# Kernel optimization log

Measured on AMD Instinct MI355X. Metric: run time of the kernel, lower is better.

## Reference

```python
import jax, jax.numpy as jnp
import numpy as np

EPS = 1e-12
NEG_SLOPE = 0.2

def _normalize(x):
    # F.normalize(x, p=2, dim=1)
    n = jnp.sqrt(jnp.sum(x * x, axis=-1, keepdims=True))
    return x / jnp.maximum(n, EPS)

def setup_inputs() -> dict:
    key = jax.random.key(0)
    ks = jax.random.split(key, 10)
    n_users, n_items, n_entities = 100000, 50000, 200000
    n_rel, n_edges, n_inter, n_hops, d = 32, 2000000, 1000000, 2, 64
    return {
        "user_emb": jax.random.normal(ks[0], (n_users, d), jnp.float32) * 0.1,
        "entity_emb": jax.random.normal(ks[1], (n_entities, d), jnp.float32) * 0.1,
        "rel_weight": jax.random.normal(ks[2], (n_rel, d), jnp.float32) * 0.1,
        "gate1_w": jax.random.normal(ks[3], (n_hops, d, d), jnp.float32) * 0.1,
        "gate2_w": jax.random.normal(ks[4], (n_hops, d, d), jnp.float32) * 0.1,
        "head": jax.random.randint(ks[5], (n_edges,), 0, n_entities, jnp.int32),
        "tail": jax.random.randint(ks[6], (n_edges,), 0, n_entities, jnp.int32),
        "edge_type": jax.random.randint(ks[7], (n_edges,), 0, n_rel, jnp.int32),
        "mat_row": jax.random.randint(ks[8], (n_inter,), 0, n_users, jnp.int32),
        "mat_col": jax.random.randint(ks[9], (n_inter,), 0, n_items, jnp.int32),
    }

def reference(user_emb, entity_emb, rel_weight, gate1_w, gate2_w,
              head, tail, edge_type, mat_row, mat_col):
    n_users = user_emb.shape[0]
    n_entities = entity_emb.shape[0]
    n_items = 50000
    n_hops = gate1_w.shape[0]

    entity_res = entity_emb
    user_res = user_emb
    for i in range(n_hops):
        # KG aggregate: gather-scale-scatter over KG triples
        msg = entity_emb[tail] * rel_weight[edge_type]          # [E, d]
        entity_agg = jax.ops.segment_sum(msg, head, num_segments=n_entities)
        # CF aggregate: user -> item
        item_neigh = user_emb[mat_row] * rel_weight[0]          # [I, d]
        i_u_agg = jax.ops.segment_sum(item_neigh, mat_col, num_segments=n_items)
        # gated fusion of KG-side and CF-side item embeddings
        ea_items = entity_agg[:n_items]
        gi = jax.nn.leaky_relu(ea_items @ gate1_w[i].T + i_u_agg @ gate2_w[i].T,
                               negative_slope=NEG_SLOPE)
        item_fusion = gi * ea_items + (1.0 - gi) * i_u_agg
        # sparse mm with binary user-item matrix == segment_sum over rows
        user_agg = jax.ops.segment_sum(item_fusion[mat_col], mat_row,
                                       num_segments=n_users)
        entity_emb = jnp.concatenate([item_fusion, entity_agg[n_items:]], axis=0)
        entity_emb = _normalize(entity_emb)
        user_emb = _normalize(user_agg)
        entity_res = entity_res + entity_emb
        user_res = user_res + user_emb
    # concatenate outputs: [n_entities + n_users, d]
    return jnp.concatenate([entity_res, user_res], axis=0)
```

## Files before the change

kernel.cpp:

```cpp
#include <hip/hip_runtime.h>
#include <hip/hip_bf16.h>

#define D 64
#define N_USERS 100000
#define N_ITEMS 50000
#define N_ENT   200000
#define EPS 1e-12f
#define CHUNK 4096
#define NBINP 512
#define CAP   8192

typedef unsigned short u16;

template<int MODE> struct Cfg;
template<> struct Cfg<0> { static constexpr int SHIFT = 9; static constexpr int NSEG = N_ENT;   };
template<> struct Cfg<1> { static constexpr int SHIFT = 7; static constexpr int NSEG = N_ITEMS; };
template<> struct Cfg<2> { static constexpr int SHIFT = 8; static constexpr int NSEG = N_USERS; };
template<int MODE> constexpr int nbin_of() {
  return (Cfg<MODE>::NSEG + (1 << Cfg<MODE>::SHIFT) - 1) >> Cfg<MODE>::SHIFT;
}

__device__ __forceinline__ float bf2f(u16 u) {
  return __uint_as_float(((unsigned)u) << 16);
}
__device__ __forceinline__ u16 f2bf(float f) {
  unsigned u = __float_as_uint(f);
  unsigned r = (u + 0x7FFFu + ((u >> 16) & 1u)) >> 16;
  return (u16)r;
}
__device__ __forceinline__ float wave_rsqnorm(float v) {
  float ss = v * v;
#pragma unroll
  for (int m = 1; m < 64; m <<= 1) ss += __shfl_xor(ss, m);
  return 1.f / fmaxf(sqrtf(ss), EPS);
}
__device__ __forceinline__ float bcast(float v, int k) {
  return __uint_as_float(__builtin_amdgcn_readlane(__float_as_uint(v), k));
}

__global__ __launch_bounds__(256) void init_embed(
    const float* __restrict__ ent, const float* __restrict__ usr,
    float* __restrict__ out_ent, float* __restrict__ out_usr,
    u16* __restrict__ ent_bf, u16* __restrict__ usr_bf) {
  int i = blockIdx.x * 256 + threadIdx.x;
  if (i < N_ENT * D) {
    float v = ent[i];
    out_ent[i] = v;
    ent_bf[i] = f2bf(v);
  }
  if (i < N_USERS * D) {
    float v = usr[i];
    out_usr[i] = v;
    usr_bf[i] = f2bf(v);
  }
}

__global__ __launch_bounds__(256) void scan_block(
    const int* __restrict__ in, int* __restrict__ out,
    int* __restrict__ bsum, int n) {
  __shared__ int sm[256];
  int tid = threadIdx.x;
  int i = blockIdx.x * 256 + tid;
  int v = (i < n) ? in[i] : 0;
  sm[tid] = v;
  __syncthreads();
  for (int ofs = 1; ofs < 256; ofs <<= 1) {
    int t = (tid >= ofs) ? sm[tid - ofs] : 0;
    __syncthreads();
    sm[tid] += t;
    __syncthreads();
  }
  if (i < n) out[i] = sm[tid] - v;
  if (tid == 255) bsum[blockIdx.x] = sm[255];
}

__global__ __launch_bounds__(1024) void scan_top(int* __restrict__ bsum, int nb) {
  __shared__ int sm[1024];
  int tid = threadIdx.x;
  int v = (tid < nb) ? bsum[tid] : 0;
  sm[tid] = v;
  __syncthreads();
  for (int ofs = 1; ofs < 1024; ofs <<= 1) {
    int t = (tid >= ofs) ? sm[tid - ofs] : 0;
    __syncthreads();
    sm[tid] += t;
    __syncthreads();
  }
  if (tid < nb) bsum[tid] = sm[tid] - v;
}

__global__ __launch_bounds__(256) void scan_addv(
    int* __restrict__ out, const int* __restrict__ bsum, int n) {
  int i = blockIdx.x * 256 + threadIdx.x;
  if (i < n) out[i] += bsum[blockIdx.x];
}

template<int MODE>
__global__ __launch_bounds__(256) void p1_hist(
    const int* __restrict__ keys, int n, int* __restrict__ bc, int nblk) {
  constexpr int SHIFT = Cfg<MODE>::SHIFT;
  constexpr int NBIN = nbin_of<MODE>();
  __shared__ int h[NBINP];
  int tid = threadIdx.x;
  h[tid] = 0; h[tid + 256] = 0;
  __syncthreads();
  int base = blockIdx.x * CHUNK;
  int end = min(base + CHUNK, n);
  for (int i = base + tid; i < end; i += 256)
    atomicAdd(&h[keys[i] >> SHIFT], 1);
  __syncthreads();
  for (int b = tid; b < NBIN; b += 256)
    bc[b * nblk + blockIdx.x] = h[b];
}

template<int MODE>
__global__ __launch_bounds__(256) void p1_scatter(
    const int* __restrict__ keys, const int* __restrict__ pa,
    const int* __restrict__ pb, int n, const int* __restrict__ sbc, int nblk,
    int2* __restrict__ out) {
  constexpr int SHIFT = Cfg<MODE>::SHIFT;
  constexpr int NBIN = nbin_of<MODE>();
  __shared__ int h[NBINP];
  __shared__ int cur[NBINP];
  __shared__ int bb[NBINP];
  __shared__ int2 staged[CHUNK];
  __shared__ int dstA[CHUNK];
  int tid = threadIdx.x;
  h[tid] = 0; h[tid + 256] = 0;
  __syncthreads();
  int base = blockIdx.x * CHUNK;
  int end = min(base + CHUNK, n);
  for (int i = base + tid; i < end; i += 256)
    atomicAdd(&h[keys[i] >> SHIFT], 1);
  __syncthreads();
  int o0 = h[tid], o1 = h[tid + 256];
  for (int ofs = 1; ofs < NBINP; ofs <<= 1) {
    int v0 = (tid >= ofs) ? h[tid - ofs] : 0;
    int v1 = (tid + 256 >= ofs) ? h[tid + 256 - ofs] : 0;
    __syncthreads();
    h[tid] += v0; h[tid + 256] += v1;
    __syncthreads();
  }
  int e0 = h[tid] - o0, e1 = h[tid + 256] - o1;
  cur[tid] = e0; cur[tid + 256] = e1;
  if (tid < NBIN)        bb[tid] = sbc[tid * nblk + blockIdx.x] - e0;
  if (tid + 256 < NBIN)  bb[tid + 256] = sbc[(tid + 256) * nblk + blockIdx.x] - e1;
  __syncthreads();
  for (int i = base + tid; i < end; i += 256) {
    int k = keys[i];
    int bin = k >> SHIFT;
    int payload;
    if constexpr (MODE == 0) payload = pa[i] | (pb[i] << 24);
    else                     payload = pa[i];
    int lp = atomicAdd(&cur[bin], 1);
    staged[lp] = make_int2(k, payload);
    dstA[lp] = bb[bin] + lp;
  }
  __syncthreads();
  int cnt = end - base;
  for (int t = tid; t < cnt; t += 256) out[dstA[t]] = staged[t];
}

template<int MODE>
__global__ __launch_bounds__(256) void p2_sort(
    const int2* __restrict__ binned, const int* __restrict__ sbc, int nblk,
    int n, int* __restrict__ vals, int* __restrict__ off) {
  constexpr int SHIFT = Cfg<MODE>::SHIFT;
  constexpr int NSEG = Cfg<MODE>::NSEG;
  constexpr int SEGBIN = 1 << SHIFT;
  constexpr int NBIN = nbin_of<MODE>();
  __shared__ int h[NBINP];
  __shared__ int cur[NBINP];
  __shared__ int staged[CAP];
  int tid = threadIdx.x;
  int b = blockIdx.x;
  int start = sbc[b * nblk];
  int endp = (b == NBIN - 1) ? n : sbc[(b + 1) * nblk];
  int cnt = endp - start;
  h[tid] = 0; h[tid + 256] = 0;
  __syncthreads();
  int segbase = b << SHIFT;
  for (int t = tid; t < cnt; t += 256)
    atomicAdd(&h[binned[start + t].x - segbase], 1);
  __syncthreads();
  int o0 = h[tid], o1 = h[tid + 256];
  for (int ofs = 1; ofs < NBINP; ofs <<= 1) {
    int v0 = (tid >= ofs) ? h[tid - ofs] : 0;
    int v1 = (tid + 256 >= ofs) ? h[tid + 256 - ofs] : 0;
    __syncthreads();
    h[tid] += v0; h[tid + 256] += v1;
    __syncthreads();
  }
  int e0 = h[tid] - o0, e1 = h[tid + 256] - o1;
  if (tid < SEGBIN && segbase + tid < NSEG) off[segbase + tid] = start + e0;
  if (tid + 256 < SEGBIN && segbase + tid + 256 < NSEG)
    off[segbase + tid + 256] = start + e1;
  if (b == NBIN - 1 && tid == 0) off[NSEG] = n;
  cur[tid] = e0; cur[tid + 256] = e1;
  __syncthreads();
  if (cnt <= CAP) {
    for (int t = tid; t < cnt; t += 256) {
      int2 e = binned[start + t];
      int lp = atomicAdd(&cur[e.x - segbase], 1);
      staged[lp] = e.y;
    }
    __syncthreads();
    for (int t = tid; t < cnt; t += 256) vals[start + t] = staged[t];
  } else {
    for (int t = tid; t < cnt; t += 256) {
      int2 e = binned[start + t];
      int lp = atomicAdd(&cur[e.x - segbase], 1);
      vals[start + lp] = e.y;
    }
  }
}

__global__ __launch_bounds__(256) void kg_gather(
    const u16* __restrict__ ent, const float* __restrict__ relw,
    const int* __restrict__ off, const int* __restrict__ pk,
    float* __restrict__ ea_items, u16* __restrict__ ent_next,
    float* __restrict__ res) {
  int h = blockIdx.x * 4 + (threadIdx.x >> 6);
  if (h >= N_ENT) return;
  int lane = threadIdx.x & 63;
  int b = off[h], e = off[h + 1];
  float acc = 0.f;
  for (int j0 = b; j0 < e; j0 += 64) {
    int cnt = min(64, e - j0);
    int p = (j0 + lane < e) ? pk[j0 + lane] : 0;
    int jj = 0;
    for (; jj + 8 <= cnt; jj += 8) {
      u16 uv[8];
      float rw[8];
#pragma unroll
      for (int k = 0; k < 8; ++k) {
        int q = __shfl(p, jj + k);
        uv[k] = ent[(q & 0xFFFFFF) * D + lane];
        rw[k] = relw[(((unsigned)q) >> 24) * D + lane];
      }
#pragma unroll
      for (int k = 0; k < 8; ++k) acc += bf2f(uv[k]) * rw[k];
    }
    for (; jj < cnt; ++jj) {
      int q = __shfl(p, jj);
      acc += bf2f(ent[(q & 0xFFFFFF) * D + lane]) *
             relw[(((unsigned)q) >> 24) * D + lane];
    }
  }
  int o = h * D + lane;
  if (h < N_ITEMS) {
    ea_items[o] = acc;
  } else {
    float nv = acc * wave_rsqnorm(acc);
    ent_next[o] = f2bf(nv);
    res[o] += nv;
  }
}

__device__ __forceinline__ float segsum_idx_bf(
    const int* __restrict__ il, int b, int e, int lane,
    const u16* __restrict__ tab) {
  float acc = 0.f;
  for (int j0 = b; j0 < e; j0 += 64) {
    int cnt = min(64, e - j0);
    int p = (j0 + lane < e) ? il[j0 + lane] : 0;
    int jj = 0;
    for (; jj + 8 <= cnt; jj += 8) {
      u16 uv[8];
#pragma unroll
      for (int k = 0; k < 8; ++k) {
        int q = __shfl(p, jj + k);
        uv[k] = tab[q * D + lane];
      }
#pragma unroll
      for (int k = 0; k < 8; ++k) acc += bf2f(uv[k]);
    }
    for (; jj < cnt; ++jj) acc += bf2f(tab[__shfl(p, jj) * D + lane]);
  }
  return acc;
}

__global__ __launch_bounds__(256) void inter_gather(
    const u16* __restrict__ usr_bf, const float* __restrict__ relw,
    const int* __restrict__ off, const int* __restrict__ vr,
    float* __restrict__ iu) {
  int c = blockIdx.x * 4 + (threadIdx.x >> 6);
  if (c >= N_ITEMS) return;
  int lane = threadIdx.x & 63;
  int b = off[c], e = off[c + 1];
  float acc = segsum_idx_bf(vr, b, e, lane, usr_bf);
  iu[c * D + lane] = acc * relw[lane];
}

__global__ __launch_bounds__(256) void fuse_items(
    const float* __restrict__ ea_items, const float* __restrict__ iu,
    const float* __restrict__ g1, const float* __restrict__ g2,
    u16* __restrict__ fus_bf, u16* __restrict__ ent_next,
    float* __restrict__ res) {
  __shared__ float G1[D][D + 1];
  __shared__ float G2[D][D + 1];
  for (int i = threadIdx.x; i < D * D; i += 256) {
    G1[i >> 6][i & 63] = g1[i];
    G2[i >> 6][i & 63] = g2[i];
  }
  __syncthreads();
  int row = blockIdx.x * 4 + (threadIdx.x >> 6);
  if (row >= N_ITEMS) return;
  int lane = threadIdx.x & 63;
  int o = row * D + lane;
  float eav = ea_items[o];
  float uv = iu[o];
  float s1 = 0.f, s2 = 0.f;
#pragma unroll
  for (int k = 0; k < D; ++k) {
    s1 += bcast(eav, k) * G1[lane][k];
    s2 += bcast(uv, k) * G2[lane][k];
  }
  float s = s1 + s2;
  float gi = s > 0.f ? s : 0.2f * s;
  float fus = gi * eav + (1.f - gi) * uv;
  fus_bf[o] = f2bf(fus);
  float nv = fus * wave_rsqnorm(fus);
  ent_next[o] = f2bf(nv);
  res[o] += nv;
}

__global__ __launch_bounds__(256) void user_gather(
    const u16* __restrict__ fus_bf, const int* __restrict__ off,
    const int* __restrict__ vc, u16* __restrict__ usr_bf,
    float* __restrict__ res) {
  int u = blockIdx.x * 4 + (threadIdx.x >> 6);
  if (u >= N_USERS) return;
  int lane = threadIdx.x & 63;
  int b = off[u], e = off[u + 1];
  float acc = segsum_idx_bf(vc, b, e, lane, fus_bf);
  float nv = acc * wave_rsqnorm(acc);
  int o = u * D + lane;
  usr_bf[o] = f2bf(nv);
  res[o] += nv;
}

template<int MODE>
static void run_sort(const int* keys, const int* pa, const int* pb, int n,
                     int2* binned, int* vals, int* off, int* bc, int* bsum,
                     hipStream_t stream) {
  constexpr int NBIN = nbin_of<MODE>();
  int nblk = (n + CHUNK - 1) / CHUNK;
  int len = NBIN * nblk;
  p1_hist<MODE><<<nblk, 256, 0, stream>>>(keys, n, bc, nblk);
  int nbs = (len + 255) / 256;
  scan_block<<<nbs, 256, 0, stream>>>(bc, bc, bsum, len);
  scan_top<<<1, 1024, 0, stream>>>(bsum, nbs);
  scan_addv<<<nbs, 256, 0, stream>>>(bc, bsum, len);
  p1_scatter<MODE><<<nblk, 256, 0, stream>>>(keys, pa, pb, n, bc, nblk, binned);
  p2_sort<MODE><<<NBIN, 256, 0, stream>>>(binned, bc, nblk, n, vals, off);
}

extern "C" void kernel_launch(void* const* d_in, const int* in_sizes, int n_in,
                              void* d_out, int out_size, void* d_ws, size_t ws_size,
                              hipStream_t stream) {
  const float* user_emb = (const float*)d_in[0];
  const float* ent_emb  = (const float*)d_in[1];
  const float* relw     = (const float*)d_in[2];
  const float* g1       = (const float*)d_in[3];
  const float* g2       = (const float*)d_in[4];
  const int*   head     = (const int*)d_in[5];
  const int*   tail     = (const int*)d_in[6];
  const int*   etype    = (const int*)d_in[7];
  const int*   mrow     = (const int*)d_in[8];
  const int*   mcol     = (const int*)d_in[9];

  const int n_edges = in_sizes[5];
  const int n_inter = in_sizes[8];
  const int n_hops  = in_sizes[3] / (D * D);

  u16* entA_bf = (u16*)d_ws;
  u16* entB_bf = entA_bf + (size_t)N_ENT * D;
  u16* usr_bf  = entB_bf + (size_t)N_ENT * D;
  u16* fus_bf  = usr_bf + (size_t)N_USERS * D;
  float* ea_items = (float*)(fus_bf + (size_t)N_ITEMS * D);
  float* iu       = ea_items + (size_t)N_ITEMS * D;
  int* ip = (int*)(iu + (size_t)N_ITEMS * D);
  int* o_head = ip;   ip += N_ENT + 1;
  int* o_col  = ip;   ip += N_ITEMS + 1;
  int* o_row  = ip;   ip += N_USERS + 1;
  int* pk_head = ip;  ip += n_edges;
  int* vr_col  = ip;  ip += n_inter;
  int* vc_row  = ip;  ip += n_inter;
  int* bc      = ip;  ip += 391 * ((n_edges + CHUNK - 1) / CHUNK) + 1;
  int* bsum    = ip;  ip += 1024;

  float* out_ent = (float*)d_out;
  float* out_usr = out_ent + (size_t)N_ENT * D;

  int2* bin_head = (int2*)d_out;
  int2* bin_col  = bin_head + n_edges;
  int2* bin_row  = bin_col + n_inter;

  run_sort<0>(head, tail, etype, n_edges, bin_head, pk_head, o_head, bc, bsum, stream);
  run_sort<1>(mcol, mrow, nullptr, n_inter, bin_col, vr_col, o_col, bc, bsum, stream);
  run_sort<2>(mrow, mcol, nullptr, n_inter, bin_row, vc_row, o_row, bc, bsum, stream);

  init_embed<<<(N_ENT * D + 255) / 256, 256, 0, stream>>>(
      ent_emb, user_emb, out_ent, out_usr, entA_bf, usr_bf);

  for (int i = 0; i < n_hops; ++i) {
    const u16* ecur = (i & 1) ? entB_bf : entA_bf;
    u16* enxt       = (i & 1) ? entA_bf : entB_bf;

    kg_gather<<<(N_ENT + 3) / 4, 256, 0, stream>>>(
        ecur, relw, o_head, pk_head, ea_items, enxt, out_ent);

    inter_gather<<<(N_ITEMS + 3) / 4, 256, 0, stream>>>(
        usr_bf, relw, o_col, vr_col, iu);

    fuse_items<<<(N_ITEMS + 3) / 4, 256, 0, stream>>>(
        ea_items, iu, g1 + (size_t)i * D * D, g2 + (size_t)i * D * D,
        fus_bf, enxt, out_ent);

    user_gather<<<(N_USERS + 3) / 4, 256, 0, stream>>>(
        fus_bf, o_row, vc_row, usr_bf, out_usr);
  }
}
```

Baseline: 607.0 us.

## Split each wave into half-waves gathering two neighbors with packed bf16x2 loads

Each gather kernel (KG, item-user, user-item) now has each half of a wave process a different neighbor row. Every lane loads a 32-bit pair of bf16 values instead of one 16-bit value, so each wave issues half as many load instructions per edge. The two halves are combined with a cross-half shuffle, and the normalisation reduction runs over 32 lanes. Only half the lanes write outputs, and odd-count tails are masked by zeroing the loaded value.

```diff
diff --git a/kernel.cpp b/kernel.cpp
--- a/kernel.cpp
+++ b/kernel.cpp
@@ -11,6 +11,7 @@
 #define CAP   8192
 
 typedef unsigned short u16;
+typedef unsigned int u32;
 
 template<int MODE> struct Cfg;
 template<> struct Cfg<0> { static constexpr int SHIFT = 9; static constexpr int NSEG = N_ENT;   };
@@ -27,12 +28,6 @@
   unsigned u = __float_as_uint(f);
   unsigned r = (u + 0x7FFFu + ((u >> 16) & 1u)) >> 16;
   return (u16)r;
-}
-__device__ __forceinline__ float wave_rsqnorm(float v) {
-  float ss = v * v;
-#pragma unroll
-  for (int m = 1; m < 64; m <<= 1) ss += __shfl_xor(ss, m);
-  return 1.f / fmaxf(sqrtf(ss), EPS);
 }
 __device__ __forceinline__ float bcast(float v, int k) {
   return __uint_as_float(__builtin_amdgcn_readlane(__float_as_uint(v), k));
@@ -216,80 +211,118 @@
 }
 
 __global__ __launch_bounds__(256) void kg_gather(
-    const u16* __restrict__ ent, const float* __restrict__ relw,
+    const u32* __restrict__ ent2, const float2* __restrict__ relw2,
     const int* __restrict__ off, const int* __restrict__ pk,
-    float* __restrict__ ea_items, u16* __restrict__ ent_next,
-    float* __restrict__ res) {
+    float2* __restrict__ ea_items2, u32* __restrict__ ent_next2,
+    float2* __restrict__ res2) {
   int h = blockIdx.x * 4 + (threadIdx.x >> 6);
   if (h >= N_ENT) return;
   int lane = threadIdx.x & 63;
+  int pi = lane & 31, half = lane >> 5;
   int b = off[h], e = off[h + 1];
-  float acc = 0.f;
+  float2 acc = {0.f, 0.f};
   for (int j0 = b; j0 < e; j0 += 64) {
     int cnt = min(64, e - j0);
     int p = (j0 + lane < e) ? pk[j0 + lane] : 0;
-    int jj = 0;
-    for (; jj + 8 <= cnt; jj += 8) {
-      u16 uv[8];
-      float rw[8];
+    int nstep = (cnt + 1) >> 1;
+    int s = 0;
+    for (; s + 8 <= nstep; s += 8) {
+      u32 raw[8];
+      float2 rw[8];
 #pragma unroll
       for (int k = 0; k < 8; ++k) {
-        int q = __shfl(p, jj + k);
-        uv[k] = ent[(q & 0xFFFFFF) * D + lane];
-        rw[k] = relw[(((unsigned)q) >> 24) * D + lane];
+        int pos = 2 * (s + k) + half;
+        int q = __shfl(p, pos);
+        raw[k] = ent2[(q & 0xFFFFFF) * 32 + pi];
+        rw[k] = relw2[(((unsigned)q) >> 24) * 32 + pi];
+        if (pos >= cnt) raw[k] = 0u;
       }
 #pragma unroll
-      for (int k = 0; k < 8; ++k) acc += bf2f(uv[k]) * rw[k];
-    }
-    for (; jj < cnt; ++jj) {
-      int q = __shfl(p, jj);
-      acc += bf2f(ent[(q & 0xFFFFFF) * D + lane]) *
-             relw[(((unsigned)q) >> 24) * D + lane];
-    }
-  }
-  int o = h * D + lane;
+      for (int k = 0; k < 8; ++k) {
+        acc.x += bf2f((u16)(raw[k] & 0xFFFF)) * rw[k].x;
+        acc.y += bf2f((u16)(raw[k] >> 16)) * rw[k].y;
+      }
+    }
+    for (; s < nstep; ++s) {
+      int pos = 2 * s + half;
+      int q = __shfl(p, pos);
+      u32 raw = ent2[(q & 0xFFFFFF) * 32 + pi];
+      float2 rw = relw2[(((unsigned)q) >> 24) * 32 + pi];
+      if (pos >= cnt) raw = 0u;
+      acc.x += bf2f((u16)(raw & 0xFFFF)) * rw.x;
+      acc.y += bf2f((u16)(raw >> 16)) * rw.y;
+    }
+  }
+  acc.x += __shfl_xor(acc.x, 32);
+  acc.y += __shfl_xor(acc.y, 32);
   if (h < N_ITEMS) {
-    ea_items[o] = acc;
+    if (half == 0) ea_items2[h * 32 + pi] = acc;
   } else {
-    float nv = acc * wave_rsqnorm(acc);
-    ent_next[o] = f2bf(nv);
-    res[o] += nv;
-  }
-}
-
-__device__ __forceinline__ float segsum_idx_bf(
-    const int* __restrict__ il, int b, int e, int lane,
-    const u16* __restrict__ tab) {
-  float acc = 0.f;
+    float ss = acc.x * acc.x + acc.y * acc.y;
+#pragma unroll
+    for (int m = 1; m < 32; m <<= 1) ss += __shfl_xor(ss, m);
+    float sc = 1.f / fmaxf(sqrtf(ss), EPS);
+    float2 nv = {acc.x * sc, acc.y * sc};
+    if (half == 0) {
+      ent_next2[h * 32 + pi] = (u32)f2bf(nv.x) | ((u32)f2bf(nv.y) << 16);
+      float2 r = res2[h * 32 + pi];
+      r.x += nv.x; r.y += nv.y;
+      res2[h * 32 + pi] = r;
+    }
+  }
+}
+
+__device__ __forceinline__ float2 segsum2_bf(
+    const int* __restrict__ il, int b, int e, int pi, int half, int lane,
+    const u32* __restrict__ tab2) {
+  float2 acc = {0.f, 0.f};
   for (int j0 = b; j0 < e; j0 += 64) {
     int cnt = min(64, e - j0);
     int p = (j0 + lane < e) ? il[j0 + lane] : 0;
-    int jj = 0;
-    for (; jj + 8 <= cnt; jj += 8) {
-      u16 uv[8];
+    int nstep = (cnt + 1) >> 1;
+    int s = 0;
+    for (; s + 8 <= nstep; s += 8) {
+      u32 raw[8];
 #pragma unroll
       for (int k = 0; k < 8; ++k) {
-        int q = __shfl(p, jj + k);
-        uv[k] = tab[q * D + lane];
+        int pos = 2 * (s + k) + half;
+        int q = __shfl(p, pos);
+        raw[k] = tab2[q * 32 + pi];
+        if (pos >= cnt) raw[k] = 0u;
       }
 #pragma unroll
-      for (int k = 0; k < 8; ++k) acc += bf2f(uv[k]);
-    }
-    for (; jj < cnt; ++jj) acc += bf2f(tab[__shfl(p, jj) * D + lane]);
-  }
+      for (int k = 0; k < 8; ++k) {
+        acc.x += bf2f((u16)(raw[k] & 0xFFFF));
+        acc.y += bf2f((u16)(raw[k] >> 16));
+      }
+    }
+    for (; s < nstep; ++s) {
+      int pos = 2 * s + half;
+      int q = __shfl(p, pos);
+      u32 raw = tab2[q * 32 + pi];
+      if (pos >= cnt) raw = 0u;
+      acc.x += bf2f((u16)(raw & 0xFFFF));
+      acc.y += bf2f((u16)(raw >> 16));
+    }
+  }
+  acc.x += __shfl_xor(acc.x, 32);
+  acc.y += __shfl_xor(acc.y, 32);
   return acc;
 }
 
 __global__ __launch_bounds__(256) void inter_gather(
-    const u16* __restrict__ usr_bf, const float* __restrict__ relw,
+    const u32* __restrict__ usr2, const float2* __restrict__ relw2,
     const int* __restrict__ off, const int* __restrict__ vr,
-    float* __restrict__ iu) {
+    float2* __restrict__ iu2) {
   int c = blockIdx.x * 4 + (threadIdx.x >> 6);
   if (c >= N_ITEMS) return;
   int lane = threadIdx.x & 63;
-  int b = off[c], e = off[c + 1];
-  float acc = segsum_idx_bf(vr, b, e, lane, usr_bf);
-  iu[c * D + lane] = acc * relw[lane];
+  int pi = lane & 31, half = lane >> 5;
+  float2 acc = segsum2_bf(vr, off[c], off[c + 1], pi, half, lane, usr2);
+  if (half == 0) {
+    float2 rw0 = relw2[pi];
+    iu2[c * 32 + pi] = make_float2(acc.x * rw0.x, acc.y * rw0.y);
+  }
 }
 
 __global__ __launch_bounds__(256) void fuse_items(
@@ -320,24 +353,34 @@
   float gi = s > 0.f ? s : 0.2f * s;
   float fus = gi * eav + (1.f - gi) * uv;
   fus_bf[o] = f2bf(fus);
-  float nv = fus * wave_rsqnorm(fus);
+  float ss = fus * fus;
+#pragma unroll
+  for (int m = 1; m < 64; m <<= 1) ss += __shfl_xor(ss, m);
+  float nv = fus / fmaxf(sqrtf(ss), EPS);
   ent_next[o] = f2bf(nv);
   res[o] += nv;
 }
 
 __global__ __launch_bounds__(256) void user_gather(
-    const u16* __restrict__ fus_bf, const int* __restrict__ off,
-    const int* __restrict__ vc, u16* __restrict__ usr_bf,
-    float* __restrict__ res) {
+    const u32* __restrict__ fus2, const int* __restrict__ off,
+    const int* __restrict__ vc, u32* __restrict__ usr2,
+    float2* __restrict__ res2) {
   int u = blockIdx.x * 4 + (threadIdx.x >> 6);
   if (u >= N_USERS) return;
   int lane = threadIdx.x & 63;
-  int b = off[u], e = off[u + 1];
-  float acc = segsum_idx_bf(vc, b, e, lane, fus_bf);
-  float nv = acc * wave_rsqnorm(acc);
-  int o = u * D + lane;
-  usr_bf[o] = f2bf(nv);
-  res[o] += nv;
+  int pi = lane & 31, half = lane >> 5;
+  float2 acc = segsum2_bf(vc, off[u], off[u + 1], pi, half, lane, fus2);
+  float ss = acc.x * acc.x + acc.y * acc.y;
+#pragma unroll
+  for (int m = 1; m < 32; m <<= 1) ss += __shfl_xor(ss, m);
+  float sc = 1.f / fmaxf(sqrtf(ss), EPS);
+  float2 nv = {acc.x * sc, acc.y * sc};
+  if (half == 0) {
+    usr2[u * 32 + pi] = (u32)f2bf(nv.x) | ((u32)f2bf(nv.y) << 16);
+    float2 r = res2[u * 32 + pi];
+    r.x += nv.x; r.y += nv.y;
+    res2[u * 32 + pi] = r;
+  }
 }
 
 template<int MODE>
@@ -409,16 +452,17 @@
     u16* enxt       = (i & 1) ? entA_bf : entB_bf;
 
     kg_gather<<<(N_ENT + 3) / 4, 256, 0, stream>>>(
-        ecur, relw, o_head, pk_head, ea_items, enxt, out_ent);
+        (const u32*)ecur, (const float2*)relw, o_head, pk_head,
+        (float2*)ea_items, (u32*)enxt, (float2*)out_ent);
 
     inter_gather<<<(N_ITEMS + 3) / 4, 256, 0, stream>>>(
-        usr_bf, relw, o_col, vr_col, iu);
+        (const u32*)usr_bf, (const float2*)relw, o_col, vr_col, (float2*)iu);
 
     fuse_items<<<(N_ITEMS + 3) / 4, 256, 0, stream>>>(
         ea_items, iu, g1 + (size_t)i * D * D, g2 + (size_t)i * D * D,
         fus_bf, enxt, out_ent);
 
     user_gather<<<(N_USERS + 3) / 4, 256, 0, stream>>>(
-        fus_bf, o_row, vc_row, usr_bf, out_usr);
-  }
-}
+        (const u32*)fus_bf, o_row, vc_row, (u32*)usr_bf, (float2*)out_usr);
+  }
+}
```

Result: no change. 612.7 us (+0.9%).

## Replace per-segment gathers with edge-balanced 64-edge windows and segmented reduction

Applied to the files above, without the earlier changes.

The CSR-row-per-wave gathers for the KG, item and user aggregations are replaced by one generic kernel. Each wave processes a fixed window of 64 sorted edges and does a segmented sum, using plain stores for segments that lie wholly inside the window and atomics for segments that cross window edges. To support this, the sort also writes per-edge segment ids, and relation weights are staged in LDS. Normalisation moves to separate fin_rows passes. The aim is full lane use and more independent loads in flight for short segments of about 10 to 20 edges, at the cost of memsets, extra fp32 raw buffers, extra kernel launches and atomics.

```diff
diff --git a/kernel.cpp b/kernel.cpp
--- a/kernel.cpp
+++ b/kernel.cpp
@@ -11,6 +11,8 @@
 #define CAP   8192
 
 typedef unsigned short u16;
+typedef unsigned int u32;
+typedef unsigned long long u64;
 
 template<int MODE> struct Cfg;
 template<> struct Cfg<0> { static constexpr int SHIFT = 9; static constexpr int NSEG = N_ENT;   };
@@ -164,7 +166,8 @@
 template<int MODE>
 __global__ __launch_bounds__(256) void p2_sort(
     const int2* __restrict__ binned, const int* __restrict__ sbc, int nblk,
-    int n, int* __restrict__ vals, int* __restrict__ off) {
+    int n, int* __restrict__ vals, int* __restrict__ hids,
+    int* __restrict__ off) {
   constexpr int SHIFT = Cfg<MODE>::SHIFT;
   constexpr int NSEG = Cfg<MODE>::NSEG;
   constexpr int SEGBIN = 1 << SHIFT;
@@ -203,6 +206,7 @@
       int2 e = binned[start + t];
       int lp = atomicAdd(&cur[e.x - segbase], 1);
       staged[lp] = e.y;
+      hids[start + lp] = e.x;
     }
     __syncthreads();
     for (int t = tid; t < cnt; t += 256) vals[start + t] = staged[t];
@@ -211,91 +215,105 @@
       int2 e = binned[start + t];
       int lp = atomicAdd(&cur[e.x - segbase], 1);
       vals[start + lp] = e.y;
+      hids[start + lp] = e.x;
     }
   }
 }
 
-__global__ __launch_bounds__(256) void kg_gather(
-    const u16* __restrict__ ent, const float* __restrict__ relw,
-    const int* __restrict__ off, const int* __restrict__ pk,
-    float* __restrict__ ea_items, u16* __restrict__ ent_next,
-    float* __restrict__ res) {
-  int h = blockIdx.x * 4 + (threadIdx.x >> 6);
-  if (h >= N_ENT) return;
+template<bool REL>
+__global__ __launch_bounds__(256) void edge_gather(
+    const u16* __restrict__ tab, const float* __restrict__ relw,
+    const int* __restrict__ pk, const int* __restrict__ hid,
+    float* __restrict__ raw, int n) {
+  __shared__ float lds_relw[REL ? 32 * D : 1];
+  if (REL) {
+    for (int i = threadIdx.x; i < 32 * D; i += 256) lds_relw[i] = relw[i];
+    __syncthreads();
+  }
+  int win = blockIdx.x * 4 + (threadIdx.x >> 6);
+  int S = win * 64;
+  if (S >= n) return;
   int lane = threadIdx.x & 63;
-  int b = off[h], e = off[h + 1];
+  int cnt = min(64, n - S);
+  int p  = (S + lane < n) ? pk[S + lane]  : 0;
+  int hd = (S + lane < n) ? hid[S + lane] : -3;
+  int hp = (S > 0) ? hid[S - 1] : -4;
+  int hn = (S + 64 < n) ? hid[S + 64] : -5;
+  int hnl = __shfl_down(hd, 1);
+  if (lane == 63) hnl = hn;
+  u64 real = __ballot(hd != hnl);
+  if (cnt < 64) real &= (1ull << cnt) - 1ull;
+  u64 emit = real | (1ull << (cnt - 1));
+  bool start_in = (__shfl(hd, 0) != hp);
   float acc = 0.f;
-  for (int j0 = b; j0 < e; j0 += 64) {
-    int cnt = min(64, e - j0);
-    int p = (j0 + lane < e) ? pk[j0 + lane] : 0;
-    int jj = 0;
-    for (; jj + 8 <= cnt; jj += 8) {
-      u16 uv[8];
-      float rw[8];
+  if (cnt == 64) {
+    for (int base = 0; base < 64; base += 8) {
+      u16 r[8]; int et[8];
 #pragma unroll
       for (int k = 0; k < 8; ++k) {
-        int q = __shfl(p, jj + k);
-        uv[k] = ent[(q & 0xFFFFFF) * D + lane];
-        rw[k] = relw[(((unsigned)q) >> 24) * D + lane];
+        int q = __shfl(p, base + k);
+        if (REL) {
+          r[k] = tab[(size_t)(q & 0xFFFFFF) * D + lane];
+          et[k] = ((unsigned)q) >> 24;
+        } else {
+          r[k] = tab[(size_t)q * D + lane];
+        }
       }
 #pragma unroll
-      for (int k = 0; k < 8; ++k) acc += bf2f(uv[k]) * rw[k];
+      for (int k = 0; k < 8; ++k) {
+        int j = base + k;
+        float c = bf2f(r[k]);
+        if (REL) c *= lds_relw[et[k] * D + lane];
+        acc += c;
+        if ((emit >> j) & 1ull) {
+          int h = __shfl(hd, j);
+          float* dst = raw + (size_t)h * D + lane;
+          if (start_in && ((real >> j) & 1ull)) *dst = acc;
+          else atomicAdd(dst, acc);
+          acc = 0.f;
+          start_in = true;
+        }
+      }
     }
-    for (; jj < cnt; ++jj) {
-      int q = __shfl(p, jj);
-      acc += bf2f(ent[(q & 0xFFFFFF) * D + lane]) *
-             relw[(((unsigned)q) >> 24) * D + lane];
+  } else {
+    for (int j = 0; j < cnt; ++j) {
+      int q = __shfl(p, j);
+      float c;
+      if (REL) c = bf2f(tab[(size_t)(q & 0xFFFFFF) * D + lane]) *
+                   lds_relw[(((unsigned)q) >> 24) * D + lane];
+      else     c = bf2f(tab[(size_t)q * D + lane]);
+      acc += c;
+      if ((emit >> j) & 1ull) {
+        int h = __shfl(hd, j);
+        float* dst = raw + (size_t)h * D + lane;
+        if (start_in && ((real >> j) & 1ull)) *dst = acc;
+        else atomicAdd(dst, acc);
+        acc = 0.f;
+        start_in = true;
+      }
     }
   }
-  int o = h * D + lane;
-  if (h < N_ITEMS) {
-    ea_items[o] = acc;
-  } else {
-    float nv = acc * wave_rsqnorm(acc);
-    ent_next[o] = f2bf(nv);
-    res[o] += nv;
-  }
-}
-
-__device__ __forceinline__ float segsum_idx_bf(
-    const int* __restrict__ il, int b, int e, int lane,
-    const u16* __restrict__ tab) {
-  float acc = 0.f;
-  for (int j0 = b; j0 < e; j0 += 64) {
-    int cnt = min(64, e - j0);
-    int p = (j0 + lane < e) ? il[j0 + lane] : 0;
-    int jj = 0;
-    for (; jj + 8 <= cnt; jj += 8) {
-      u16 uv[8];
-#pragma unroll
-      for (int k = 0; k < 8; ++k) {
-        int q = __shfl(p, jj + k);
-        uv[k] = tab[q * D + lane];
-      }
-#pragma unroll
-      for (int k = 0; k < 8; ++k) acc += bf2f(uv[k]);
-    }
-    for (; jj < cnt; ++jj) acc += bf2f(tab[__shfl(p, jj) * D + lane]);
-  }
-  return acc;
-}
-
-__global__ __launch_bounds__(256) void inter_gather(
-    const u16* __restrict__ usr_bf, const float* __restrict__ relw,
-    const int* __restrict__ off, const int* __restrict__ vr,
-    float* __restrict__ iu) {
-  int c = blockIdx.x * 4 + (threadIdx.x >> 6);
-  if (c >= N_ITEMS) return;
+}
+
+__global__ __launch_bounds__(256) void fin_rows(
+    const float* __restrict__ raw, u16* __restrict__ out_bf,
+    float* __restrict__ res, int row0, int nrows) {
+  int r = blockIdx.x * 4 + (threadIdx.x >> 6);
+  if (r >= nrows) return;
+  int row = row0 + r;
   int lane = threadIdx.x & 63;
-  int b = off[c], e = off[c + 1];
-  float acc = segsum_idx_bf(vr, b, e, lane, usr_bf);
-  iu[c * D + lane] = acc * relw[lane];
+  size_t o = (size_t)row * D + lane;
+  float v = raw[o];
+  float nv = v * wave_rsqnorm(v);
+  out_bf[o] = f2bf(nv);
+  res[o] += nv;
 }
 
 __global__ __launch_bounds__(256) void fuse_items(
-    const float* __restrict__ ea_items, const float* __restrict__ iu,
+    const float* __restrict__ ent_raw, const float* __restrict__ iu,
+    const float* __restrict__ relw,
     const float* __restrict__ g1, const float* __restrict__ g2,
-    u16* __restrict__ fus_bf, u16* __restrict__ ent_next,
+    u16* __restrict__ fus_bf, u16* __restrict__ ent_bf,
     float* __restrict__ res) {
   __shared__ float G1[D][D + 1];
   __shared__ float G2[D][D + 1];
@@ -307,9 +325,9 @@
   int row = blockIdx.x * 4 + (threadIdx.x >> 6);
   if (row >= N_ITEMS) return;
   int lane = threadIdx.x & 63;
-  int o = row * D + lane;
-  float eav = ea_items[o];
-  float uv = iu[o];
+  size_t o = (size_t)row * D + lane;
+  float eav = ent_raw[o];
+  float uv = iu[o] * relw[lane];
   float s1 = 0.f, s2 = 0.f;
 #pragma unroll
   for (int k = 0; k < D; ++k) {
@@ -321,29 +339,14 @@
   float fus = gi * eav + (1.f - gi) * uv;
   fus_bf[o] = f2bf(fus);
   float nv = fus * wave_rsqnorm(fus);
-  ent_next[o] = f2bf(nv);
-  res[o] += nv;
-}
-
-__global__ __launch_bounds__(256) void user_gather(
-    const u16* __restrict__ fus_bf, const int* __restrict__ off,
-    const int* __restrict__ vc, u16* __restrict__ usr_bf,
-    float* __restrict__ res) {
-  int u = blockIdx.x * 4 + (threadIdx.x >> 6);
-  if (u >= N_USERS) return;
-  int lane = threadIdx.x & 63;
-  int b = off[u], e = off[u + 1];
-  float acc = segsum_idx_bf(vc, b, e, lane, fus_bf);
-  float nv = acc * wave_rsqnorm(acc);
-  int o = u * D + lane;
-  usr_bf[o] = f2bf(nv);
+  ent_bf[o] = f2bf(nv);
   res[o] += nv;
 }
 
 template<int MODE>
 static void run_sort(const int* keys, const int* pa, const int* pb, int n,
-                     int2* binned, int* vals, int* off, int* bc, int* bsum,
-                     hipStream_t stream) {
+                     int2* binned, int* vals, int* hids, int* off, int* bc,
+                     int* bsum, hipStream_t stream) {
   constexpr int NBIN = nbin_of<MODE>();
   int nblk = (n + CHUNK - 1) / CHUNK;
   int len = NBIN * nblk;
@@ -353,7 +356,7 @@
   scan_top<<<1, 1024, 0, stream>>>(bsum, nbs);
   scan_addv<<<nbs, 256, 0, stream>>>(bc, bsum, len);
   p1_scatter<MODE><<<nblk, 256, 0, stream>>>(keys, pa, pb, n, bc, nblk, binned);
-  p2_sort<MODE><<<NBIN, 256, 0, stream>>>(binned, bc, nblk, n, vals, off);
+  p2_sort<MODE><<<NBIN, 256, 0, stream>>>(binned, bc, nblk, n, vals, hids, off);
 }
 
 extern "C" void kernel_launch(void* const* d_in, const int* in_sizes, int n_in,
@@ -374,20 +377,23 @@
   const int n_inter = in_sizes[8];
   const int n_hops  = in_sizes[3] / (D * D);
 
-  u16* entA_bf = (u16*)d_ws;
-  u16* entB_bf = entA_bf + (size_t)N_ENT * D;
-  u16* usr_bf  = entB_bf + (size_t)N_ENT * D;
-  u16* fus_bf  = usr_bf + (size_t)N_USERS * D;
-  float* ea_items = (float*)(fus_bf + (size_t)N_ITEMS * D);
-  float* iu       = ea_items + (size_t)N_ITEMS * D;
-  int* ip = (int*)(iu + (size_t)N_ITEMS * D);
+  u16* ent_bf = (u16*)d_ws;
+  u16* usr_bf = ent_bf + (size_t)N_ENT * D;
+  u16* fus_bf = usr_bf + (size_t)N_USERS * D;
+  float* ent_raw = (float*)(fus_bf + (size_t)N_ITEMS * D);
+  float* usr_raw = ent_raw + (size_t)N_ENT * D;
+  float* iu      = usr_raw;
+  int* ip = (int*)(usr_raw + (size_t)N_USERS * D);
   int* o_head = ip;   ip += N_ENT + 1;
   int* o_col  = ip;   ip += N_ITEMS + 1;
   int* o_row  = ip;   ip += N_USERS + 1;
   int* pk_head = ip;  ip += n_edges;
+  int* hid_h   = ip;  ip += n_edges;
   int* vr_col  = ip;  ip += n_inter;
+  int* hid_c   = ip;  ip += n_inter;
   int* vc_row  = ip;  ip += n_inter;
-  int* bc      = ip;  ip += 391 * ((n_edges + CHUNK - 1) / CHUNK) + 1;
+  int* hid_r   = ip;  ip += n_inter;
+  int* bc      = ip;  ip += 391 * ((n_edges + CHUNK - 1) / CHUNK) + 64;
   int* bsum    = ip;  ip += 1024;
 
   float* out_ent = (float*)d_out;
@@ -397,28 +403,41 @@
   int2* bin_col  = bin_head + n_edges;
   int2* bin_row  = bin_col + n_inter;
 
-  run_sort<0>(head, tail, etype, n_edges, bin_head, pk_head, o_head, bc, bsum, stream);
-  run_sort<1>(mcol, mrow, nullptr, n_inter, bin_col, vr_col, o_col, bc, bsum, stream);
-  run_sort<2>(mrow, mcol, nullptr, n_inter, bin_row, vc_row, o_row, bc, bsum, stream);
+  run_sort<0>(head, tail, etype, n_edges, bin_head, pk_head, hid_h, o_head,
+              bc, bsum, stream);
+  run_sort<1>(mcol, mrow, nullptr, n_inter, bin_col, vr_col, hid_c, o_col,
+              bc, bsum, stream);
+  run_sort<2>(mrow, mcol, nullptr, n_inter, bin_row, vc_row, hid_r, o_row,
+              bc, bsum, stream);
 
   init_embed<<<(N_ENT * D + 255) / 256, 256, 0, stream>>>(
-      ent_emb, user_emb, out_ent, out_usr, entA_bf, usr_bf);
+      ent_emb, user_emb, out_ent, out_usr, ent_bf, usr_bf);
+
+  const int nwin_kg = (n_edges + 63) / 64;
+  const int nwin_in = (n_inter + 63) / 64;
 
   for (int i = 0; i < n_hops; ++i) {
-    const u16* ecur = (i & 1) ? entB_bf : entA_bf;
-    u16* enxt       = (i & 1) ? entA_bf : entB_bf;
-
-    kg_gather<<<(N_ENT + 3) / 4, 256, 0, stream>>>(
-        ecur, relw, o_head, pk_head, ea_items, enxt, out_ent);
-
-    inter_gather<<<(N_ITEMS + 3) / 4, 256, 0, stream>>>(
-        usr_bf, relw, o_col, vr_col, iu);
+    hipMemsetAsync(ent_raw, 0, (size_t)N_ENT * D * sizeof(float), stream);
+    hipMemsetAsync(iu, 0, (size_t)N_ITEMS * D * sizeof(float), stream);
+
+    edge_gather<true><<<(nwin_kg + 3) / 4, 256, 0, stream>>>(
+        ent_bf, relw, pk_head, hid_h, ent_raw, n_edges);
+
+    edge_gather<false><<<(nwin_in + 3) / 4, 256, 0, stream>>>(
+        usr_bf, nullptr, vr_col, hid_c, iu, n_inter);
 
     fuse_items<<<(N_ITEMS + 3) / 4, 256, 0, stream>>>(
-        ea_items, iu, g1 + (size_t)i * D * D, g2 + (size_t)i * D * D,
-        fus_bf, enxt, out_ent);
-
-    user_gather<<<(N_USERS + 3) / 4, 256, 0, stream>>>(
-        fus_bf, o_row, vc_row, usr_bf, out_usr);
-  }
-}
+        ent_raw, iu, relw, g1 + (size_t)i * D * D, g2 + (size_t)i * D * D,
+        fus_bf, ent_bf, out_ent);
+
+    fin_rows<<<(N_ENT - N_ITEMS + 3) / 4, 256, 0, stream>>>(
+        ent_raw, ent_bf, out_ent, N_ITEMS, N_ENT - N_ITEMS);
+
+    hipMemsetAsync(usr_raw, 0, (size_t)N_USERS * D * sizeof(float), stream);
+    edge_gather<false><<<(nwin_in + 3) / 4, 256, 0, stream>>>(
+        fus_bf, nullptr, vc_row, hid_r, usr_raw, n_inter);
+
+    fin_rows<<<(N_USERS + 3) / 4, 256, 0, stream>>>(
+        usr_raw, usr_bf, out_usr, 0, N_USERS);
+  }
+}
```

Measured after the change: 588.8 us. 1.03x faster.
